# Performance work log

Hardware: AMD Instinct MI355X
Metric: run time of the kernel (lower is better)

The kernel has to match this reference:

```python
import jax, jax.numpy as jnp
import numpy as np

D_MODEL = 2048
N_HEADS = 16
D_K = D_MODEL // N_HEADS
D_FF = 5504
SEQ = 4096
CONTEXT_LENGTH = 4096
THETA = 10000.0
EPS = 1e-5


def _linear(x, w):
    # w: (out, in), matches torch einsum '...i,oi->...o'
    return jnp.einsum('...i,oi->...o', x, w)


def _rmsnorm(x, g):
    xf = x.astype(jnp.float32)
    rms = jnp.sqrt(jnp.mean(xf * xf, axis=-1, keepdims=True) + EPS)
    return (xf / rms * g).astype(x.dtype)


def _rope_tables():
    powers = jnp.arange(0, D_K, 2, dtype=jnp.float32) / D_K
    freqs = 1.0 / (THETA ** powers)                       # (D_K/2,)
    t = jnp.arange(CONTEXT_LENGTH, dtype=jnp.float32)
    ang = jnp.outer(t, freqs)                             # (ctx, D_K/2)
    return jnp.cos(ang), jnp.sin(ang)


def _apply_rope(x, token_positions, cos_c, sin_c):
    # x: (b, h, s, d_k); token_positions: (b, s)
    cos = cos_c[token_positions][None].astype(x.dtype)    # (1, b, s, d_k/2)
    sin = sin_c[token_positions][None].astype(x.dtype)
    x_even = x[..., ::2]
    x_odd = x[..., 1::2]
    r1 = x_even * cos - x_odd * sin
    r2 = x_even * sin + x_odd * cos
    # interleave back: (..., d_k/2, 2) -> (..., d_k)
    out = jnp.stack([r1, r2], axis=-1)
    return out.reshape(x.shape)


def setup_inputs() -> dict:
    key = jax.random.key(0)
    ks = jax.random.split(key, 12)

    def w(k, out_f, in_f):
        std = (2.0 / (in_f + out_f)) ** 0.5
        return std * jax.random.normal(k, (out_f, in_f), dtype=jnp.float32)

    return {
        'x': jax.random.normal(ks[0], (1, SEQ, D_MODEL), dtype=jnp.float32),
        'w_q': w(ks[1], D_MODEL, D_MODEL),
        'w_k': w(ks[2], D_MODEL, D_MODEL),
        'w_v': w(ks[3], D_MODEL, D_MODEL),
        'w_o': w(ks[4], D_MODEL, D_MODEL),
        'w1': w(ks[5], D_FF, D_MODEL),
        'w2': w(ks[6], D_MODEL, D_FF),
        'w3': w(ks[7], D_FF, D_MODEL),
        'g1': jnp.ones((D_MODEL,), dtype=jnp.float32),
        'g2': jnp.ones((D_MODEL,), dtype=jnp.float32),
        'token_positions': jnp.broadcast_to(jnp.arange(SEQ, dtype=jnp.int32)[None, :], (1, SEQ)),
    }


def reference(x, w_q, w_k, w_v, w_o, w1, w2, w3, g1, g2, token_positions):
    b, s, _ = x.shape
    cos_c, sin_c = _rope_tables()

    # --- pre-norm attention ---
    xn = _rmsnorm(x, g1)
    def heads(t):
        return t.reshape(b, s, N_HEADS, D_K).transpose(0, 2, 1, 3)  # (b,h,s,d)
    q = heads(_linear(xn, w_q))
    k = heads(_linear(xn, w_k))
    v = heads(_linear(xn, w_v))
    q = _apply_rope(q, token_positions, cos_c, sin_c)
    k = _apply_rope(k, token_positions, cos_c, sin_c)

    score = jnp.einsum('bhqd,bhkd->bhqk', q, k) / (D_K ** 0.5)
    causal = jnp.tril(jnp.ones((s, s), dtype=bool))
    score = jnp.where(causal, score, -jnp.inf)
    probs = jax.nn.softmax(score, axis=-1)
    attn = jnp.einsum('bhqk,bhkd->bhqd', probs, v)
    attn = attn.transpose(0, 2, 1, 3).reshape(b, s, D_MODEL)
    x = x + _linear(attn, w_o)

    # --- pre-norm SwiGLU FFN ---
    xn = _rmsnorm(x, g2)
    gate = _linear(xn, w1)
    gate = gate * jax.nn.sigmoid(gate)  # SiLU
    x = x + _linear(gate * _linear(xn, w3), w2)
    return x
```

## Files before the change

### kernel.cpp

```cpp
#include <hip/hip_runtime.h>
#include <hip/hip_bf16.h>
#include <cstdint>
#include <cstddef>

constexpr int S_   = 4096;
constexpr int DM   = 2048;
constexpr int NH   = 16;
constexpr int DK   = 128;
constexpr int DFF  = 5504;
constexpr int DFFP = 5632;
constexpr int QLD  = 3 * DM;

typedef float  f32x4  __attribute__((ext_vector_type(4)));
typedef float  f32x16 __attribute__((ext_vector_type(16)));
typedef short  s16x8  __attribute__((ext_vector_type(8)));
typedef __bf16 bfx8   __attribute__((ext_vector_type(8)));

template <typename T, typename U>
__device__ inline auto mfma_try(T a, T b, f32x4 c, int)
    -> decltype(__builtin_amdgcn_mfma_f32_16x16x32_bf16(a, b, c, 0, 0, 0)) {
  return __builtin_amdgcn_mfma_f32_16x16x32_bf16(a, b, c, 0, 0, 0);
}
template <typename T, typename U>
__device__ inline f32x4 mfma_try(T a, T b, f32x4 c, long) {
  U a2 = __builtin_bit_cast(U, a);
  U b2 = __builtin_bit_cast(U, b);
  return __builtin_amdgcn_mfma_f32_16x16x32_bf16(a2, b2, c, 0, 0, 0);
}
__device__ __forceinline__ f32x4 MFMA_BF16(s16x8 a, s16x8 b, f32x4 c) {
  return mfma_try<s16x8, bfx8>(a, b, c, 0);
}

template <typename T, typename U>
__device__ inline auto mfma32_try(T a, T b, f32x16 c, int)
    -> decltype(__builtin_amdgcn_mfma_f32_32x32x16_bf16(a, b, c, 0, 0, 0)) {
  return __builtin_amdgcn_mfma_f32_32x32x16_bf16(a, b, c, 0, 0, 0);
}
template <typename T, typename U>
__device__ inline f32x16 mfma32_try(T a, T b, f32x16 c, long) {
  U a2 = __builtin_bit_cast(U, a);
  U b2 = __builtin_bit_cast(U, b);
  return __builtin_amdgcn_mfma_f32_32x32x16_bf16(a2, b2, c, 0, 0, 0);
}
__device__ __forceinline__ f32x16 MFMA32(s16x8 a, s16x8 b, f32x16 c) {
  return mfma32_try<s16x8, bfx8>(a, b, c, 0);
}

__device__ __forceinline__ void async_ld16(void* lds, const void* g) {
  __builtin_amdgcn_global_load_lds(
      (__attribute__((address_space(1))) void*)(g),
      (__attribute__((address_space(3))) void*)(lds), 16, 0, 0);
}

__device__ __forceinline__ float bf2f(__hip_bfloat16 h) { return __bfloat162float(h); }
__device__ __forceinline__ __hip_bfloat16 f2bf(float f) { return __float2bfloat16(f); }

__global__ __launch_bounds__(256) void cvt_kernel(const float* __restrict__ in,
                                                  __hip_bfloat16* __restrict__ out, int n) {
  int i = (blockIdx.x * 256 + threadIdx.x) * 4;
  if (i >= n) return;
  float4 v = *reinterpret_cast<const float4*>(in + i);
  union { __hip_bfloat16 h[4]; uint2 u; } pk;
  pk.h[0] = f2bf(v.x); pk.h[1] = f2bf(v.y); pk.h[2] = f2bf(v.z); pk.h[3] = f2bf(v.w);
  *reinterpret_cast<uint2*>(out + i) = pk.u;
}

__global__ __launch_bounds__(256) void cvt3_kernel(const float* __restrict__ a,
                                                   const float* __restrict__ b,
                                                   const float* __restrict__ c,
                                                   __hip_bfloat16* __restrict__ out, int n) {
  int i = (blockIdx.x * 256 + threadIdx.x) * 4;
  if (i >= 3 * n) return;
  const float* src = (i < n) ? (a + i) : (i < 2 * n) ? (b + i - n) : (c + i - 2 * n);
  float4 v = *reinterpret_cast<const float4*>(src);
  union { __hip_bfloat16 h[4]; uint2 u; } pk;
  pk.h[0] = f2bf(v.x); pk.h[1] = f2bf(v.y); pk.h[2] = f2bf(v.z); pk.h[3] = f2bf(v.w);
  *reinterpret_cast<uint2*>(out + i) = pk.u;
}

__global__ __launch_bounds__(256) void cvt_swiglu(const float* __restrict__ w1,
                                                  const float* __restrict__ w3,
                                                  __hip_bfloat16* __restrict__ out) {
  const size_t i = ((size_t)blockIdx.x * 256 + threadIdx.x) * 4;
  const int br = (int)(i >> 11);
  const int k  = (int)(i & 2047);
  const int g  = br >> 5, j = br & 31;
  const int srow = g * 16 + (j & 15);
  union { __hip_bfloat16 h[4]; uint2 u; } pk;
  if (srow < DFF) {
    const float* src = (j < 16 ? w1 : w3) + (size_t)srow * DM + k;
    float4 v = *reinterpret_cast<const float4*>(src);
    pk.h[0] = f2bf(v.x); pk.h[1] = f2bf(v.y); pk.h[2] = f2bf(v.z); pk.h[3] = f2bf(v.w);
  } else {
    pk.u.x = 0u; pk.u.y = 0u;
  }
  *reinterpret_cast<uint2*>(out + i) = pk.u;
}

__global__ __launch_bounds__(256) void rmsnorm_kernel(const float* __restrict__ x,
                                                      const float* __restrict__ g,
                                                      __hip_bfloat16* __restrict__ out) {
  const int row = blockIdx.x, tid = threadIdx.x;
  const float4* xr = reinterpret_cast<const float4*>(x + (size_t)row * DM);
  float4 a = xr[tid], b = xr[tid + 256];
  float ss = a.x*a.x + a.y*a.y + a.z*a.z + a.w*a.w
           + b.x*b.x + b.y*b.y + b.z*b.z + b.w*b.w;
#pragma unroll
  for (int off = 1; off < 64; off <<= 1) ss += __shfl_xor(ss, off);
  __shared__ float red[4];
  if ((tid & 63) == 0) red[tid >> 6] = ss;
  __syncthreads();
  const float inv = rsqrtf((red[0] + red[1] + red[2] + red[3]) * (1.0f / DM) + 1e-5f);
  const float4* gr = reinterpret_cast<const float4*>(g);
  float4 ga = gr[tid], gb = gr[tid + 256];
  union { __hip_bfloat16 h[4]; uint2 u; } pa, pb;
  pa.h[0] = f2bf(a.x * inv * ga.x); pa.h[1] = f2bf(a.y * inv * ga.y);
  pa.h[2] = f2bf(a.z * inv * ga.z); pa.h[3] = f2bf(a.w * inv * ga.w);
  pb.h[0] = f2bf(b.x * inv * gb.x); pb.h[1] = f2bf(b.y * inv * gb.y);
  pb.h[2] = f2bf(b.z * inv * gb.z); pb.h[3] = f2bf(b.w * inv * gb.w);
  uint2* o = reinterpret_cast<uint2*>(out + (size_t)row * DM);
  o[tid] = pa.u; o[tid + 256] = pb.u;
}

__global__ __launch_bounds__(256) void rope_kernel(__hip_bfloat16* __restrict__ t,
                                                   const int* __restrict__ pos) {
  const size_t idx = (size_t)blockIdx.x * 256 + threadIdx.x;
  const int j = (int)(idx & 63);
  const int h = (int)((idx >> 6) & 15);
  const int s = (int)(idx >> 10);
  const float p = (float)pos[s];
  const float freq = exp2f((float)j * (-13.287712379549449f / 64.0f));
  float sn, cs;
  sincosf(p * freq, &sn, &cs);
  const float cl2 = 1.4426950408889634f * 0.08838834764831845f;
  __hip_bfloat16* ptrQ = t + (size_t)s * QLD + h * DK + 2 * j;
  __hip_bfloat16* ptrK = ptrQ + DM;
  {
    const float e = bf2f(ptrQ[0]), o = bf2f(ptrQ[1]);
    ptrQ[0] = f2bf((e * cs - o * sn) * cl2);
    ptrQ[1] = f2bf((e * sn + o * cs) * cl2);
  }
  {
    const float e = bf2f(ptrK[0]), o = bf2f(ptrK[1]);
    ptrK[0] = f2bf(e * cs - o * sn);
    ptrK[1] = f2bf(e * sn + o * cs);
  }
}

__global__ __launch_bounds__(256) void transpose_v(const __hip_bfloat16* __restrict__ qkv,
                                                   __hip_bfloat16* __restrict__ vt) {
  __shared__ __hip_bfloat16 tile[64][65];
  const int h = blockIdx.z;
  const int s0 = blockIdx.x * 64, d0 = blockIdx.y * 64;
  const int lane = threadIdx.x & 63, w = threadIdx.x >> 6;
#pragma unroll
  for (int i = 0; i < 16; i++) {
    const int r = w * 16 + i;
    tile[r][lane] = qkv[(size_t)(s0 + r) * QLD + 2 * DM + h * DK + d0 + lane];
  }
  __syncthreads();
#pragma unroll
  for (int i = 0; i < 16; i++) {
    const int r = w * 16 + i;
    vt[(size_t)(h * DK + d0 + r) * S_ + s0 + lane] = tile[lane][r];
  }
}

enum { EP_BF16 = 0, EP_SILU = 1, EP_MUL = 2, EP_ADDF32 = 3, EP_SWIGLU = 4 };

template <int EP>
__global__ __launch_bounds__(512, 2) void gemm2(const __hip_bfloat16* __restrict__ A,
                                                const __hip_bfloat16* __restrict__ B,
                                                int N, int K, int lda, int ldb,
                                                void* outp, const void* extra) {
  __shared__ char lds[3][24576];
  const int tid = threadIdx.x;
  const int wave = tid >> 6, lane = tid & 63;
  const int l15 = lane & 15, l4 = lane >> 4;
  const int wm = wave >> 2, wn = wave & 3;

  const int nbn = gridDim.x;
  const int nwg = gridDim.x * gridDim.y;
  int lin = blockIdx.y * gridDim.x + blockIdx.x;
  if ((nwg & 7) == 0) lin = (lin & 7) * (nwg >> 3) + (lin >> 3);
  const int bm = (lin / nbn) * 128;
  const int bn = (lin % nbn) * 256;

  const int NT = K >> 5;

  const int srcCh = ((tid & 3) ^ ((tid >> 3) & 3)) * 16;
  const char* Asrc  = (const char*)A + (size_t)(bm + (tid >> 2)) * lda * 2 + srcCh;
  const char* Bsrc0 = (const char*)B + (size_t)(bn + (tid >> 2)) * ldb * 2 + srcCh;
  const char* Bsrc1 = (const char*)B + (size_t)(bn + 128 + (tid >> 2)) * ldb * 2 + srcCh;
  char* const ldsA  = &lds[0][0] + wave * 1024;
  char* const ldsB0 = &lds[0][0] + 8192 + wave * 1024;
  char* const ldsB1 = &lds[0][0] + 16384 + wave * 1024;

  auto stage_a  = [&](int t, int s) { async_ld16(ldsA  + s * 24576, Asrc  + (size_t)t * 64); };
  auto stage_b0 = [&](int t, int s) { async_ld16(ldsB0 + s * 24576, Bsrc0 + (size_t)t * 64); };
  auto stage_b1 = [&](int t, int s) { async_ld16(ldsB1 + s * 24576, Bsrc1 + (size_t)t * 64); };

  const int rdch = (l4 ^ ((l15 >> 1) & 3)) * 16;
  auto rd_a = [&](int s, int mq, int f) -> s16x8 {
    return *(const s16x8*)(&lds[s][0] + (wm * 64 + mq * 32 + f * 16 + l15) * 64 + rdch);
  };
  auto rd_b = [&](int s, int nf) -> s16x8 {
    return *(const s16x8*)(&lds[s][8192] + (wn * 64 + nf * 16 + l15) * 64 + rdch);
  };

  f32x4 acc[4][4] = {};

  stage_a(0, 0); stage_b0(0, 0); stage_b1(0, 0);
  stage_a(1, 1); stage_b0(1, 1); stage_b1(1, 1);

  for (int t = 0; t < NT; t++) {
    const int s = t % 3;
    if (t + 1 < NT) { asm volatile("s_waitcnt vmcnt(3)" ::: "memory"); }
    else            { asm volatile("s_waitcnt vmcnt(0)" ::: "memory"); }
    __builtin_amdgcn_s_barrier();
    asm volatile("" ::: "memory");
    s16x8 b0 = rd_b(s, 0), b1 = rd_b(s, 1), b2 = rd_b(s, 2), b3 = rd_b(s, 3);
    s16x8 a0 = rd_a(s, 0, 0), a1 = rd_a(s, 0, 1);
    if (t + 2 < NT) { const int s2 = (t + 2) % 3; stage_a(t + 2, s2); stage_b0(t + 2, s2); }
    __builtin_amdgcn_s_barrier();
    asm volatile("" ::: "memory");
    __builtin_amdgcn_s_setprio(1);
    acc[0][0] = MFMA_BF16(a0, b0, acc[0][0]);
    acc[0][1] = MFMA_BF16(a0, b1, acc[0][1]);
    acc[0][2] = MFMA_BF16(a0, b2, acc[0][2]);
    acc[0][3] = MFMA_BF16(a0, b3, acc[0][3]);
    acc[1][0] = MFMA_BF16(a1, b0, acc[1][0]);
    acc[1][1] = MFMA_BF16(a1, b1, acc[1][1]);
    acc[1][2] = MFMA_BF16(a1, b2, acc[1][2]);
    acc[1][3] = MFMA_BF16(a1, b3, acc[1][3]);
    __builtin_amdgcn_s_setprio(0);
    s16x8 a2 = rd_a(s, 1, 0), a3 = rd_a(s, 1, 1);
    if (t + 2 < NT) stage_b1(t + 2, (t + 2) % 3);
    __builtin_amdgcn_s_barrier();
    asm volatile("" ::: "memory");
    __builtin_amdgcn_s_setprio(1);
    acc[2][0] = MFMA_BF16(a2, b0, acc[2][0]);
    acc[2][1] = MFMA_BF16(a2, b1, acc[2][1]);
    acc[2][2] = MFMA_BF16(a2, b2, acc[2][2]);
    acc[2][3] = MFMA_BF16(a2, b3, acc[2][3]);
    acc[3][0] = MFMA_BF16(a3, b0, acc[3][0]);
    acc[3][1] = MFMA_BF16(a3, b1, acc[3][1]);
    acc[3][2] = MFMA_BF16(a3, b2, acc[3][2]);
    acc[3][3] = MFMA_BF16(a3, b3, acc[3][3]);
    __builtin_amdgcn_s_setprio(0);
  }

  if constexpr (EP == EP_SWIGLU) {
#pragma unroll
    for (int mf = 0; mf < 4; mf++)
#pragma unroll
      for (int pp = 0; pp < 2; pp++)
#pragma unroll
        for (int r = 0; r < 4; r++) {
          const int row = bm + wm * 64 + mf * 16 + l4 * 4 + r;
          const int col = (bn >> 1) + wn * 32 + pp * 16 + l15;
          const float gt = acc[mf][pp * 2][r];
          const float up = acc[mf][pp * 2 + 1][r];
          ((__hip_bfloat16*)outp)[(size_t)row * N + col] =
              f2bf(gt / (1.0f + __expf(-gt)) * up);
        }
    return;
  }

#pragma unroll
  for (int mf = 0; mf < 4; mf++)
#pragma unroll
    for (int nf = 0; nf < 4; nf++)
#pragma unroll
      for (int r = 0; r < 4; r++) {
        const int row = bm + wm * 64 + mf * 16 + l4 * 4 + r;
        const int col = bn + wn * 64 + nf * 16 + l15;
        const size_t idx = (size_t)row * N + col;
        const float v = acc[mf][nf][r];
        if constexpr (EP == EP_BF16) {
          ((__hip_bfloat16*)outp)[idx] = f2bf(v);
        } else if constexpr (EP == EP_SILU) {
          ((__hip_bfloat16*)outp)[idx] = f2bf(v / (1.0f + __expf(-v)));
        } else if constexpr (EP == EP_MUL) {
          const float o = bf2f(((const __hip_bfloat16*)extra)[idx]);
          ((__hip_bfloat16*)outp)[idx] = f2bf(v * o);
        } else {
          ((float*)outp)[idx] = v + ((const float*)extra)[idx];
        }
      }
}

__global__ __launch_bounds__(256, 2) void attn_kernel(const __hip_bfloat16* __restrict__ qkv,
                                                      const __hip_bfloat16* __restrict__ vt,
                                                      __hip_bfloat16* __restrict__ out) {
  __shared__ char sK[2][64 * 256];
  __shared__ char sV[2][128 * 128];

  const int h = blockIdx.y;
  int qt = (blockIdx.x + 2 * (h & 7)) & 31;
  if (h >= 8) qt = 31 - qt;
  const int qtile = qt;
  const int q0 = qtile * 128;
  const int tid = threadIdx.x, wave = tid >> 6, lane = tid & 63;
  const int l31 = lane & 31, hi = lane >> 5;
  const int qr = q0 + wave * 32 + l31;
  const int ntiles = qtile * 2 + 2;

  s16x8 qf[8];
  {
    const char* qsrc = (const char*)qkv + (size_t)qr * (QLD * 2) + h * DK * 2 + hi * 16;
#pragma unroll
    for (int s = 0; s < 8; s++) qf[s] = *(const s16x8*)(qsrc + s * 32);
  }

  const char* qkvK = (const char*)qkv + ((size_t)DM + h * DK) * 2;
  const char* vtH  = (const char*)vt + (size_t)h * DK * S_ * 2;

  auto stage_K = [&](int t, int buf) {
    const int kv0 = t * 64;
#pragma unroll
    for (int a = 0; a < 4; a++) {
      const int rl = wave * 16 + a * 4 + (lane >> 4);
      const int ck = (lane & 15) ^ (rl & 7);
      async_ld16(sK[buf] + (wave * 16 + a * 4) * 256,
                 qkvK + (size_t)(kv0 + rl) * (QLD * 2) + ck * 16);
    }
  };
  auto stage_V = [&](int t, int buf) {
    const int kv0 = t * 64;
#pragma unroll
    for (int a = 0; a < 4; a++) {
      const int rl = wave * 32 + a * 8 + (lane >> 3);
      const int cv = (lane & 7) ^ (rl & 7);
      async_ld16(sV[buf] + (wave * 32 + a * 8) * 128,
                 vtH + ((size_t)rl * S_ + kv0) * 2 + cv * 16);
    }
  };

  f32x16 acc[4] = {};
  float m_ = -__builtin_inff(), l_ = 0.f;

  stage_K(0, 0);
  stage_V(0, 0);

  int buf = 0;
  for (int t = 0; t < ntiles; t++) {
    if (t + 1 < ntiles) {
      stage_K(t + 1, buf ^ 1);
      stage_V(t + 1, buf ^ 1);
      asm volatile("s_waitcnt vmcnt(8)" ::: "memory");
    } else {
      asm volatile("s_waitcnt vmcnt(0)" ::: "memory");
    }
    __builtin_amdgcn_s_barrier();

    const char* Kt = sK[buf];
    const char* Vt = sV[buf];

    f32x16 st0 = {}, st1 = {};
    __builtin_amdgcn_s_setprio(1);
#pragma unroll
    for (int s = 0; s < 8; s++) {
      const int cc = s * 2 + hi;
      const int cs = (cc & 8) | ((cc ^ l31) & 7);
      s16x8 k0 = *(const s16x8*)(Kt + l31 * 256 + cs * 16);
      s16x8 k1 = *(const s16x8*)(Kt + (32 + l31) * 256 + cs * 16);
      st0 = MFMA32(k0, qf[s], st0);
      st1 = MFMA32(k1, qf[s], st1);
    }
    __builtin_amdgcn_s_setprio(0);

    const int kvb = t * 64;
    float p[32];
    float mx = -__builtin_inff();
    if (kvb + 63 <= q0 + wave * 32) {
#pragma unroll
      for (int r = 0; r < 16; r++) {
        p[r]      = st0[r];
        p[16 + r] = st1[r];
        mx = fmaxf(mx, fmaxf(p[r], p[16 + r]));
      }
    } else {
#pragma unroll
      for (int r = 0; r < 16; r++) {
        const int kv = kvb + (r & 3) + 8 * (r >> 2) + 4 * hi;
        p[r]      = (kv <= qr)      ? st0[r] : -__builtin_inff();
        p[16 + r] = (kv + 32 <= qr) ? st1[r] : -__builtin_inff();
        mx = fmaxf(mx, fmaxf(p[r], p[16 + r]));
      }
    }
    mx = fmaxf(mx, __shfl_xor(mx, 32));
    const bool skip = __all(mx - m_ <= 8.0f);
    float alpha = 1.0f;
    if (!skip) {
      const float nm = fmaxf(m_, mx);
      alpha = exp2f(m_ - nm);
      m_ = nm;
#pragma unroll
      for (int dt = 0; dt < 4; dt++)
#pragma unroll
        for (int r = 0; r < 16; r++) acc[dt][r] *= alpha;
    }
    float psum = 0.f;
#pragma unroll
    for (int i = 0; i < 32; i++) {
      p[i] = exp2f(p[i] - m_);
      psum += p[i];
    }
    psum += __shfl_xor(psum, 32);
    l_ = l_ * alpha + psum;

    unsigned ps[16];
#pragma unroll
    for (int h2 = 0; h2 < 2; h2++)
#pragma unroll
      for (int t2 = 0; t2 < 4; t2++)
#pragma unroll
        for (int rp = 0; rp < 2; rp++) {
          union { __hip_bfloat16 hh[2]; unsigned u; } pk;
          pk.hh[0] = f2bf(p[h2 * 16 + t2 * 4 + rp * 2]);
          pk.hh[1] = f2bf(p[h2 * 16 + t2 * 4 + rp * 2 + 1]);
          ps[h2 * 8 + t2 * 2 + rp] = pk.u;
        }

#pragma unroll
    for (int s = 0; s < 4; s++) {
      const int h2 = s >> 1;
      const int iA = h2 * 8 + (2 * (s & 1)) * 2;
      const int iB = h2 * 8 + (2 * (s & 1) + 1) * 2;
      const unsigned keep0 = hi ? ps[iB]     : ps[iA];
      const unsigned keep1 = hi ? ps[iB + 1] : ps[iA + 1];
      const unsigned send0 = hi ? ps[iA]     : ps[iB];
      const unsigned send1 = hi ? ps[iA + 1] : ps[iB + 1];
      const unsigned recv0 = __shfl_xor(send0, 32);
      const unsigned recv1 = __shfl_xor(send1, 32);
      union { unsigned u[4]; s16x8 v; } fr;
      fr.u[0] = hi ? recv0 : keep0;
      fr.u[1] = hi ? recv1 : keep1;
      fr.u[2] = hi ? keep0 : recv0;
      fr.u[3] = hi ? keep1 : recv1;
      const s16x8 pa = fr.v;
      __builtin_amdgcn_s_setprio(1);
#pragma unroll
      for (int dt = 0; dt < 4; dt++) {
        s16x8 vf = *(const s16x8*)(Vt + (dt * 32 + l31) * 128 +
                                   (((s * 2 + hi) ^ (l31 & 7)) & 7) * 16);
        acc[dt] = MFMA32(vf, pa, acc[dt]);
      }
      __builtin_amdgcn_s_setprio(0);
    }

    if (t + 2 < ntiles) __builtin_amdgcn_s_barrier();
    buf ^= 1;
  }

  const float rl = 1.0f / l_;
  __hip_bfloat16* orow = out + (size_t)qr * DM + h * DK;
#pragma unroll
  for (int dt = 0; dt < 4; dt++)
#pragma unroll
    for (int rq = 0; rq < 4; rq++) {
      union { __hip_bfloat16 hh[4]; uint2 u; } pk;
#pragma unroll
      for (int e = 0; e < 4; e++) pk.hh[e] = f2bf(acc[dt][rq * 4 + e] * rl);
      *reinterpret_cast<uint2*>(orow + dt * 32 + 8 * rq + 4 * hi) = pk.u;
    }
}

extern "C" void kernel_launch(void* const* d_in, const int* in_sizes, int n_in,
                              void* d_out, int out_size, void* d_ws, size_t ws_size,
                              hipStream_t stream) {
  const float* x   = (const float*)d_in[0];
  const float* w_q = (const float*)d_in[1];
  const float* w_k = (const float*)d_in[2];
  const float* w_v = (const float*)d_in[3];
  const float* w_o = (const float*)d_in[4];
  const float* w1  = (const float*)d_in[5];
  const float* w2  = (const float*)d_in[6];
  const float* w3  = (const float*)d_in[7];
  const float* g1  = (const float*)d_in[8];
  const float* g2  = (const float*)d_in[9];
  const int*   tp  = (const int*)d_in[10];
  float* outf = (float*)d_out;

  constexpr size_t SZ_WQKV  = (size_t)3 * DM * DM * 2;
  constexpr size_t OFF_ATTN = (size_t)DM * DM * 2;
  constexpr size_t OFF_XN   = SZ_WQKV;
  constexpr size_t OFF_A2   = OFF_XN + (size_t)S_ * DM * 2;
  constexpr size_t OFF_VT   = OFF_A2 + (size_t)S_ * QLD * 2;
  constexpr size_t WS_NEED  = OFF_VT + (size_t)NH * DK * S_ * 2;
  constexpr size_t OFF_WF   = (size_t)S_ * DM * 2;
  constexpr size_t OFF_FF1  = OFF_WF + (size_t)2 * DFFP * DM * 2;
  static_assert(OFF_FF1 + (size_t)S_ * DFFP * 2 == WS_NEED, "ws layout");
  if (ws_size < WS_NEED) return;

  char* base = (char*)d_ws;
  __hip_bfloat16* warena = (__hip_bfloat16*)base;
  __hip_bfloat16* attnb  = (__hip_bfloat16*)(base + OFF_ATTN);
  __hip_bfloat16* xn     = (__hip_bfloat16*)(base + OFF_XN);
  __hip_bfloat16* qkv    = (__hip_bfloat16*)(base + OFF_A2);
  __hip_bfloat16* vt     = (__hip_bfloat16*)(base + OFF_VT);
  __hip_bfloat16* xn2    = (__hip_bfloat16*)base;
  __hip_bfloat16* wfused = (__hip_bfloat16*)(base + OFF_WF);
  __hip_bfloat16* ff1    = (__hip_bfloat16*)(base + OFF_FF1);

  const int nwq = DM * DM;

  cvt3_kernel<<<(3 * nwq) / 1024, 256, 0, stream>>>(w_q, w_k, w_v, warena, nwq);
  rmsnorm_kernel<<<S_, 256, 0, stream>>>(x, g1, xn);
  gemm2<EP_BF16><<<dim3(QLD / 256, S_ / 128), 512, 0, stream>>>(xn, warena, QLD, DM, DM, DM, qkv, nullptr);
  rope_kernel<<<(S_ * NH * 64) / 256, 256, 0, stream>>>(qkv, tp);
  transpose_v<<<dim3(S_ / 64, DK / 64, NH), 256, 0, stream>>>(qkv, vt);
  attn_kernel<<<dim3(S_ / 128, NH), 256, 0, stream>>>(qkv, vt, attnb);
  cvt_kernel<<<nwq / 1024, 256, 0, stream>>>(w_o, warena, nwq);
  gemm2<EP_ADDF32><<<dim3(DM / 256, S_ / 128), 512, 0, stream>>>(attnb, warena, DM, DM, DM, DM, outf, x);

  rmsnorm_kernel<<<S_, 256, 0, stream>>>(outf, g2, xn2);
  cvt_swiglu<<<(2 * DFFP * DM) / 1024, 256, 0, stream>>>(w1, w3, wfused);
  gemm2<EP_SWIGLU><<<dim3((2 * DFFP) / 256, S_ / 128), 512, 0, stream>>>(xn2, wfused, DFFP, DM, DM, DM, ff1, nullptr);
  cvt_kernel<<<(DM * DFF) / 1024, 256, 0, stream>>>(w2, warena, DM * DFF);
  gemm2<EP_ADDF32><<<dim3(DM / 256, S_ / 128), 512, 0, stream>>>(ff1, warena, DM, DFF, DFFP, DFF, outf, outf);
}
```

Before: 741.9 us.

## Add 256x256 four-stage GEMM for QKV and SwiGLU, drop mid-loop barriers

Adds a gemm4 kernel that computes a 256x256 output tile per 512-thread block. Each wave accumulates 8x4 MFMA fragments, and a 4-slot, 128KB LDS ring prefetches three K-steps ahead. The QKV projection and the fused SwiGLU up-projection now use it to raise operand reuse and cut global traffic per FLOP. The remaining gemm2 drops its two intra-iteration barriers and its unused SwiGLU epilogue. Trade-offs: one block per CU, fewer blocks leaving partial tail waves on the grid, and looser wave synchronization in gemm2.

```diff
diff --git a/kernel.cpp b/kernel.cpp
--- a/kernel.cpp
+++ b/kernel.cpp
@@ -222,8 +222,6 @@
     s16x8 b0 = rd_b(s, 0), b1 = rd_b(s, 1), b2 = rd_b(s, 2), b3 = rd_b(s, 3);
     s16x8 a0 = rd_a(s, 0, 0), a1 = rd_a(s, 0, 1);
     if (t + 2 < NT) { const int s2 = (t + 2) % 3; stage_a(t + 2, s2); stage_b0(t + 2, s2); }
-    __builtin_amdgcn_s_barrier();
-    asm volatile("" ::: "memory");
     __builtin_amdgcn_s_setprio(1);
     acc[0][0] = MFMA_BF16(a0, b0, acc[0][0]);
     acc[0][1] = MFMA_BF16(a0, b1, acc[0][1]);
@@ -236,8 +234,6 @@
     __builtin_amdgcn_s_setprio(0);
     s16x8 a2 = rd_a(s, 1, 0), a3 = rd_a(s, 1, 1);
     if (t + 2 < NT) stage_b1(t + 2, (t + 2) % 3);
-    __builtin_amdgcn_s_barrier();
-    asm volatile("" ::: "memory");
     __builtin_amdgcn_s_setprio(1);
     acc[2][0] = MFMA_BF16(a2, b0, acc[2][0]);
     acc[2][1] = MFMA_BF16(a2, b1, acc[2][1]);
@@ -248,23 +244,6 @@
     acc[3][2] = MFMA_BF16(a3, b2, acc[3][2]);
     acc[3][3] = MFMA_BF16(a3, b3, acc[3][3]);
     __builtin_amdgcn_s_setprio(0);
-  }
-
-  if constexpr (EP == EP_SWIGLU) {
-#pragma unroll
-    for (int mf = 0; mf < 4; mf++)
-#pragma unroll
-      for (int pp = 0; pp < 2; pp++)
-#pragma unroll
-        for (int r = 0; r < 4; r++) {
-          const int row = bm + wm * 64 + mf * 16 + l4 * 4 + r;
-          const int col = (bn >> 1) + wn * 32 + pp * 16 + l15;
-          const float gt = acc[mf][pp * 2][r];
-          const float up = acc[mf][pp * 2 + 1][r];
-          ((__hip_bfloat16*)outp)[(size_t)row * N + col] =
-              f2bf(gt / (1.0f + __expf(-gt)) * up);
-        }
-    return;
   }
 
 #pragma unroll
@@ -286,6 +265,152 @@
           ((__hip_bfloat16*)outp)[idx] = f2bf(v * o);
         } else {
           ((float*)outp)[idx] = v + ((const float*)extra)[idx];
+        }
+      }
+}
+
+template <int EP>
+__global__ __launch_bounds__(512, 1) void gemm4(const __hip_bfloat16* __restrict__ A,
+                                                const __hip_bfloat16* __restrict__ B,
+                                                int N, int K, int lda, int ldb,
+                                                void* outp, const void* extra) {
+  __shared__ char lds[4][32768];
+  const int tid = threadIdx.x;
+  const int wave = tid >> 6, lane = tid & 63;
+  const int l15 = lane & 15, l4 = lane >> 4;
+  const int wm = wave >> 2, wn = wave & 3;
+
+  const int nbn = gridDim.x;
+  const int nwg = gridDim.x * gridDim.y;
+  int lin = blockIdx.y * gridDim.x + blockIdx.x;
+  if ((nwg & 7) == 0) lin = (lin & 7) * (nwg >> 3) + (lin >> 3);
+  const int bm = (lin / nbn) * 256;
+  const int bn = (lin % nbn) * 256;
+
+  const int NT = K >> 5;
+
+  const int srcCh = ((tid & 3) ^ ((tid >> 3) & 3)) * 16;
+  const char* Asrc0 = (const char*)A + (size_t)(bm + (tid >> 2)) * lda * 2 + srcCh;
+  const char* Asrc1 = (const char*)A + (size_t)(bm + 128 + (tid >> 2)) * lda * 2 + srcCh;
+  const char* Bsrc0 = (const char*)B + (size_t)(bn + (tid >> 2)) * ldb * 2 + srcCh;
+  const char* Bsrc1 = (const char*)B + (size_t)(bn + 128 + (tid >> 2)) * ldb * 2 + srcCh;
+  char* const ldsA0 = &lds[0][0] + wave * 1024;
+  char* const ldsA1 = &lds[0][0] + 8192 + wave * 1024;
+  char* const ldsB0 = &lds[0][0] + 16384 + wave * 1024;
+  char* const ldsB1 = &lds[0][0] + 24576 + wave * 1024;
+
+  auto stage_a0 = [&](int t, int s) { async_ld16(ldsA0 + s * 32768, Asrc0 + (size_t)t * 64); };
+  auto stage_a1 = [&](int t, int s) { async_ld16(ldsA1 + s * 32768, Asrc1 + (size_t)t * 64); };
+  auto stage_b0 = [&](int t, int s) { async_ld16(ldsB0 + s * 32768, Bsrc0 + (size_t)t * 64); };
+  auto stage_b1 = [&](int t, int s) { async_ld16(ldsB1 + s * 32768, Bsrc1 + (size_t)t * 64); };
+
+  const int rdch = (l4 ^ ((l15 >> 1) & 3)) * 16;
+  auto rd_a = [&](int s, int mf) -> s16x8 {
+    return *(const s16x8*)(&lds[s][0] + (wm * 128 + mf * 16 + l15) * 64 + rdch);
+  };
+  auto rd_b = [&](int s, int nf) -> s16x8 {
+    return *(const s16x8*)(&lds[s][16384] + (wn * 64 + nf * 16 + l15) * 64 + rdch);
+  };
+
+  f32x4 acc[8][4] = {};
+
+#pragma unroll
+  for (int t = 0; t < 3; t++) {
+    stage_a0(t, t); stage_a1(t, t); stage_b0(t, t); stage_b1(t, t);
+  }
+
+  for (int t = 0; t < NT; t++) {
+    const int s = t & 3;
+    if (t + 1 < NT) { asm volatile("s_waitcnt vmcnt(8)" ::: "memory"); }
+    else            { asm volatile("s_waitcnt vmcnt(0)" ::: "memory"); }
+    __builtin_amdgcn_s_barrier();
+    asm volatile("" ::: "memory");
+    const int s3 = (t + 3) & 3;
+    const bool pf = (t + 3 < NT);
+    s16x8 b0 = rd_b(s, 0), b1 = rd_b(s, 1), b2 = rd_b(s, 2), b3 = rd_b(s, 3);
+    s16x8 a0 = rd_a(s, 0), a1 = rd_a(s, 1);
+    if (pf) stage_a0(t + 3, s3);
+    __builtin_amdgcn_s_setprio(1);
+    acc[0][0] = MFMA_BF16(a0, b0, acc[0][0]);
+    acc[0][1] = MFMA_BF16(a0, b1, acc[0][1]);
+    acc[0][2] = MFMA_BF16(a0, b2, acc[0][2]);
+    acc[0][3] = MFMA_BF16(a0, b3, acc[0][3]);
+    acc[1][0] = MFMA_BF16(a1, b0, acc[1][0]);
+    acc[1][1] = MFMA_BF16(a1, b1, acc[1][1]);
+    acc[1][2] = MFMA_BF16(a1, b2, acc[1][2]);
+    acc[1][3] = MFMA_BF16(a1, b3, acc[1][3]);
+    __builtin_amdgcn_s_setprio(0);
+    s16x8 a2 = rd_a(s, 2), a3 = rd_a(s, 3);
+    if (pf) stage_a1(t + 3, s3);
+    __builtin_amdgcn_s_setprio(1);
+    acc[2][0] = MFMA_BF16(a2, b0, acc[2][0]);
+    acc[2][1] = MFMA_BF16(a2, b1, acc[2][1]);
+    acc[2][2] = MFMA_BF16(a2, b2, acc[2][2]);
+    acc[2][3] = MFMA_BF16(a2, b3, acc[2][3]);
+    acc[3][0] = MFMA_BF16(a3, b0, acc[3][0]);
+    acc[3][1] = MFMA_BF16(a3, b1, acc[3][1]);
+    acc[3][2] = MFMA_BF16(a3, b2, acc[3][2]);
+    acc[3][3] = MFMA_BF16(a3, b3, acc[3][3]);
+    __builtin_amdgcn_s_setprio(0);
+    s16x8 a4 = rd_a(s, 4), a5 = rd_a(s, 5);
+    if (pf) stage_b0(t + 3, s3);
+    __builtin_amdgcn_s_setprio(1);
+    acc[4][0] = MFMA_BF16(a4, b0, acc[4][0]);
+    acc[4][1] = MFMA_BF16(a4, b1, acc[4][1]);
+    acc[4][2] = MFMA_BF16(a4, b2, acc[4][2]);
+    acc[4][3] = MFMA_BF16(a4, b3, acc[4][3]);
+    acc[5][0] = MFMA_BF16(a5, b0, acc[5][0]);
+    acc[5][1] = MFMA_BF16(a5, b1, acc[5][1]);
+    acc[5][2] = MFMA_BF16(a5, b2, acc[5][2]);
+    acc[5][3] = MFMA_BF16(a5, b3, acc[5][3]);
+    __builtin_amdgcn_s_setprio(0);
+    s16x8 a6 = rd_a(s, 6), a7 = rd_a(s, 7);
+    if (pf) stage_b1(t + 3, s3);
+    __builtin_amdgcn_s_setprio(1);
+    acc[6][0] = MFMA_BF16(a6, b0, acc[6][0]);
+    acc[6][1] = MFMA_BF16(a6, b1, acc[6][1]);
+    acc[6][2] = MFMA_BF16(a6, b2, acc[6][2]);
+    acc[6][3] = MFMA_BF16(a6, b3, acc[6][3]);
+    acc[7][0] = MFMA_BF16(a7, b0, acc[7][0]);
+    acc[7][1] = MFMA_BF16(a7, b1, acc[7][1]);
+    acc[7][2] = MFMA_BF16(a7, b2, acc[7][2]);
+    acc[7][3] = MFMA_BF16(a7, b3, acc[7][3]);
+    __builtin_amdgcn_s_setprio(0);
+  }
+
+  if constexpr (EP == EP_SWIGLU) {
+#pragma unroll
+    for (int mf = 0; mf < 8; mf++)
+#pragma unroll
+      for (int pp = 0; pp < 2; pp++)
+#pragma unroll
+        for (int r = 0; r < 4; r++) {
+          const int row = bm + wm * 128 + mf * 16 + l4 * 4 + r;
+          const int col = (bn >> 1) + wn * 32 + pp * 16 + l15;
+          const float gt = acc[mf][pp * 2][r];
+          const float up = acc[mf][pp * 2 + 1][r];
+          ((__hip_bfloat16*)outp)[(size_t)row * N + col] =
+              f2bf(gt / (1.0f + __expf(-gt)) * up);
+        }
+    return;
+  }
+
+#pragma unroll
+  for (int mf = 0; mf < 8; mf++)
+#pragma unroll
+    for (int nf = 0; nf < 4; nf++)
+#pragma unroll
+      for (int r = 0; r < 4; r++) {
+        const int row = bm + wm * 128 + mf * 16 + l4 * 4 + r;
+        const int col = bn + wn * 64 + nf * 16 + l15;
+        const size_t idx = (size_t)row * N + col;
+        const float v = acc[mf][nf][r];
+        if constexpr (EP == EP_BF16) {
+          ((__hip_bfloat16*)outp)[idx] = f2bf(v);
+        } else if constexpr (EP == EP_ADDF32) {
+          ((float*)outp)[idx] = v + ((const float*)extra)[idx];
+        } else {
+          ((__hip_bfloat16*)outp)[idx] = f2bf(v);
         }
       }
 }
@@ -508,7 +633,7 @@
 
   cvt3_kernel<<<(3 * nwq) / 1024, 256, 0, stream>>>(w_q, w_k, w_v, warena, nwq);
   rmsnorm_kernel<<<S_, 256, 0, stream>>>(x, g1, xn);
-  gemm2<EP_BF16><<<dim3(QLD / 256, S_ / 128), 512, 0, stream>>>(xn, warena, QLD, DM, DM, DM, qkv, nullptr);
+  gemm4<EP_BF16><<<dim3(QLD / 256, S_ / 256), 512, 0, stream>>>(xn, warena, QLD, DM, DM, DM, qkv, nullptr);
   rope_kernel<<<(S_ * NH * 64) / 256, 256, 0, stream>>>(qkv, tp);
   transpose_v<<<dim3(S_ / 64, DK / 64, NH), 256, 0, stream>>>(qkv, vt);
   attn_kernel<<<dim3(S_ / 128, NH), 256, 0, stream>>>(qkv, vt, attnb);
@@ -517,7 +642,7 @@
 
   rmsnorm_kernel<<<S_, 256, 0, stream>>>(outf, g2, xn2);
   cvt_swiglu<<<(2 * DFFP * DM) / 1024, 256, 0, stream>>>(w1, w3, wfused);
-  gemm2<EP_SWIGLU><<<dim3((2 * DFFP) / 256, S_ / 128), 512, 0, stream>>>(xn2, wfused, DFFP, DM, DM, DM, ff1, nullptr);
+  gemm4<EP_SWIGLU><<<dim3((2 * DFFP) / 256, S_ / 256), 512, 0, stream>>>(xn2, wfused, DFFP, DM, DM, DM, ff1, nullptr);
   cvt_kernel<<<(DM * DFF) / 1024, 256, 0, stream>>>(w2, warena, DM * DFF);
   gemm2<EP_ADDF32><<<dim3(DM / 256, S_ / 128), 512, 0, stream>>>(ff1, warena, DM, DFF, DFFP, DFF, outf, outf);
 }
```

Result: faster. 695.6 us (-6.3%).
